# Kernel tuning notes

Hardware: AMD Instinct MI355X
Metric: run time of the kernel (lower is better)

Reference implementation:

```python
import jax, jax.numpy as jnp
import numpy as np

N_NODES = 100000
N_EDGES = 1600000
IN_CH = 256
OUT_CH = 32
HEADS = 4
NEG_SLOPE = 0.2


def setup_inputs() -> dict:
    key = jax.random.key(0)
    k1, k2, k3, k4, k5 = jax.random.split(key, 5)
    x = jax.random.normal(k1, (N_NODES, IN_CH), dtype=jnp.float32)
    edge_index = jax.random.randint(k2, (2, N_EDGES), 0, N_NODES, dtype=jnp.int64)
    hc = HEADS * OUT_CH
    # glorot init like the torch module
    std_w = np.sqrt(6.0 / (hc + IN_CH))
    W = jax.random.uniform(k3, (hc, IN_CH), dtype=jnp.float32, minval=-std_w, maxval=std_w)
    b = jnp.zeros((hc,), dtype=jnp.float32)
    std_a = np.sqrt(6.0 / (hc + 2))
    att = jax.random.uniform(k4, (hc, 2), dtype=jnp.float32, minval=-std_a, maxval=std_a)
    return {"x": x, "edge_index": edge_index, "W": W, "b": b, "att": att}


def reference(x, edge_index, W, b, att):
    # flow = 'target_to_source': tid=0, sid=1
    tar = edge_index[0]
    src = edge_index[1]
    feat = x @ W.T + b                      # [N, H*C]
    e_pre = feat @ att                      # [N, 2]
    e_src = e_pre[:, 0:1]                   # [N, 1]
    e_tar = e_pre[:, 1:2]                   # [N, 1]
    # edge scores
    e = jnp.exp(jax.nn.leaky_relu(e_src[src] + e_tar[tar], negative_slope=NEG_SLOPE))   # [E, 1]
    e_self = jnp.exp(jax.nn.leaky_relu(e_src + e_tar, negative_slope=NEG_SLOPE))        # [N, 1]
    # softmax denominator over incoming edges + self loop
    e_sum = jax.ops.segment_sum(e, tar, num_segments=N_NODES) + e_self                  # [N, 1]
    alpha_self = e_self / e_sum             # [N, 1]
    alpha = e / e_sum[tar]                  # [E, 1]
    # weighted aggregation (dropout=0 / eval -> identity)
    out = jax.ops.segment_sum(feat[src] * alpha, tar, num_segments=N_NODES)
    out = out + feat * alpha_self           # [N, H*C], concat=True
    return out
```

## Files before the change

kernel.cpp:

```cpp
#include <hip/hip_runtime.h>
#include <hip/hip_bf16.h>
#include <math.h>

#define N_NODES 100000
#define N_EDGES 1600000
#define IN_CH 256
#define HC 128
#define NEG_SLOPE 0.2f

#define NB_C 196
#define CCAP 8704
#define CHUNK 3200

typedef __attribute__((ext_vector_type(8))) short short8;
typedef __attribute__((ext_vector_type(4))) float floatx4;

__device__ inline ushort f2b(float f) {
    __hip_bfloat16 h = __float2bfloat16(f);
    return *(ushort*)&h;
}

#define GBM 128

__global__ __launch_bounds__(256, 2)
void gemm_mfma(const float* __restrict__ x, const float* __restrict__ W,
               const float* __restrict__ b, const float* __restrict__ att,
               __hip_bfloat16* __restrict__ featb,
               float* __restrict__ e_src, float* __restrict__ e_tar,
               float* __restrict__ e_self) {
    __shared__ ushort xs[128][72];
    __shared__ ushort wsh[128][72];

    const int tid  = threadIdx.x;
    const int wave = tid >> 6;
    const int lane = tid & 63;
    const int l16  = lane >> 4;
    const int lc   = lane & 15;
    const int row0 = blockIdx.x * GBM;

    floatx4 acc[2][8];
    #pragma unroll
    for (int mt = 0; mt < 2; ++mt)
        #pragma unroll
        for (int nt = 0; nt < 8; ++nt)
            acc[mt][nt] = (floatx4){0.f, 0.f, 0.f, 0.f};

    for (int kb = 0; kb < 4; ++kb) {
        const int r  = tid >> 4;
        const int kq = tid & 15;
        #pragma unroll
        for (int i = 0; i < 8; ++i) {
            int rr = r + i * 16;
            int gr = row0 + rr;
            float4 v = make_float4(0.f, 0.f, 0.f, 0.f);
            if (gr < N_NODES)
                v = *(const float4*)&x[(size_t)gr * IN_CH + kb * 64 + kq * 4];
            ushort4 u;
            u.x = f2b(v.x); u.y = f2b(v.y); u.z = f2b(v.z); u.w = f2b(v.w);
            *(ushort4*)&xs[rr][kq * 4] = u;
        }
        #pragma unroll
        for (int i = 0; i < 8; ++i) {
            int rr = r + i * 16;
            float4 v = *(const float4*)&W[(size_t)rr * IN_CH + kb * 64 + kq * 4];
            ushort4 u;
            u.x = f2b(v.x); u.y = f2b(v.y); u.z = f2b(v.z); u.w = f2b(v.w);
            *(ushort4*)&wsh[rr][kq * 4] = u;
        }
        __syncthreads();
        #pragma unroll
        for (int ks = 0; ks < 2; ++ks) {
            short8 a0 = *(short8*)&xs[wave * 32 + lc][ks * 32 + l16 * 8];
            short8 a1 = *(short8*)&xs[wave * 32 + 16 + lc][ks * 32 + l16 * 8];
            short8 bf[8];
            #pragma unroll
            for (int nt = 0; nt < 8; ++nt)
                bf[nt] = *(short8*)&wsh[nt * 16 + lc][ks * 32 + l16 * 8];
            #pragma unroll
            for (int nt = 0; nt < 8; ++nt) {
                acc[0][nt] = __builtin_amdgcn_mfma_f32_16x16x32_bf16(a0, bf[nt], acc[0][nt], 0, 0, 0);
                acc[1][nt] = __builtin_amdgcn_mfma_f32_16x16x32_bf16(a1, bf[nt], acc[1][nt], 0, 0, 0);
            }
        }
        __syncthreads();
    }

    float av0[8], av1[8], bc[8];
    #pragma unroll
    for (int nt = 0; nt < 8; ++nt) {
        float2 av = *(const float2*)&att[(nt * 16 + lc) * 2];
        av0[nt] = av.x; av1[nt] = av.y;
        bc[nt] = b[nt * 16 + lc];
    }

    #pragma unroll
    for (int mt = 0; mt < 2; ++mt) {
        #pragma unroll
        for (int rg = 0; rg < 4; ++rg) {
            int row = row0 + wave * 32 + mt * 16 + l16 * 4 + rg;
            float s = 0.f, t = 0.f;
            float vals[8];
            #pragma unroll
            for (int nt = 0; nt < 8; ++nt) {
                float v = acc[mt][nt][rg] + bc[nt];
                vals[nt] = v;
                s += v * av0[nt];
                t += v * av1[nt];
            }
            #pragma unroll
            for (int off = 8; off; off >>= 1) {
                s += __shfl_xor(s, off);
                t += __shfl_xor(t, off);
            }
            if (row < N_NODES) {
                if (lc == 0) {
                    e_src[row] = s;
                    e_tar[row] = t;
                    float z = s + t;
                    float lr = z > 0.f ? z : NEG_SLOPE * z;
                    e_self[row] = __expf(lr);
                }
                #pragma unroll
                for (int nt = 0; nt < 8; ++nt)
                    featb[(size_t)row * HC + nt * 16 + lc] = __float2bfloat16(vals[nt]);
            }
        }
    }
}

__global__ __launch_bounds__(256)
void bin2_k(const int* __restrict__ ei, int* __restrict__ gcur,
            int* __restrict__ ebuf) {
    __shared__ int lcnt[NB_C];
    __shared__ int lcur[NB_C];
    const int base = blockIdx.x * CHUNK;

    for (int i = threadIdx.x; i < NB_C; i += 256) lcnt[i] = 0;
    __syncthreads();

    for (int i = threadIdx.x; i < CHUNK; i += 256)
        atomicAdd(&lcnt[ei[base + i] >> 9], 1);
    __syncthreads();

    for (int bkt = threadIdx.x; bkt < NB_C; bkt += 256) {
        int c = lcnt[bkt];
        lcur[bkt] = c ? atomicAdd(&gcur[bkt], c) : 0;
    }
    __syncthreads();

    for (int i = threadIdx.x; i < CHUNK; i += 256) {
        int t = ei[base + i];
        int s = ei[N_EDGES + base + i];
        int bkt = t >> 9;
        int pos = atomicAdd(&lcur[bkt], 1);
        if (pos < CCAP)
            ebuf[bkt * CCAP + pos] = s | ((t & 511) << 17);
    }
}

__global__ __launch_bounds__(512)
void bucket_csr2_k(const int* __restrict__ gcur, const int* __restrict__ ebuf,
                   int* __restrict__ offsets, int* __restrict__ csr_src) {
    const int b = blockIdx.x;
    const int tid = threadIdx.x;

    __shared__ int sc[256];
    __shared__ int lcnt[512];
    __shared__ int lofs[512];
    __shared__ int lout[CCAP];

    if (tid < 256) {
        int c = 0;
        if (tid < NB_C) { c = gcur[tid]; if (c > CCAP) c = CCAP; }
        sc[tid] = c;
    }
    lcnt[tid] = 0;
    __syncthreads();
    #pragma unroll
    for (int off = 1; off < 256; off <<= 1) {
        int v = 0;
        if (tid < 256) v = sc[tid] + ((tid >= off) ? sc[tid - off] : 0);
        __syncthreads();
        if (tid < 256) sc[tid] = v;
        __syncthreads();
    }
    int count = gcur[b]; if (count > CCAP) count = CCAP;
    const int base = (b == 0) ? 0 : sc[b - 1];

    const int* st = &ebuf[b * CCAP];
    for (int i = tid; i < count; i += 512)
        atomicAdd(&lcnt[st[i] >> 17], 1);
    __syncthreads();

    lofs[tid] = lcnt[tid];
    __syncthreads();
    for (int off = 1; off < 512; off <<= 1) {
        int v = lofs[tid] + ((tid >= off) ? lofs[tid - off] : 0);
        __syncthreads();
        lofs[tid] = v;
        __syncthreads();
    }
    int excl = lofs[tid] - lcnt[tid];
    lcnt[tid] = excl;

    {
        int n0 = b * 512 + tid;
        if (n0 < N_NODES) offsets[n0] = base + excl;
    }
    if (b == NB_C - 1 && tid == 0) offsets[N_NODES] = base + count;
    __syncthreads();

    for (int i = tid; i < count; i += 512) {
        int v = st[i];
        int pos = atomicAdd(&lcnt[v >> 17], 1);
        lout[pos] = v & 0x1FFFF;
    }
    __syncthreads();

    for (int i = tid; i < count; i += 512)
        csr_src[base + i] = lout[i];
}

__device__ inline float edge_e(float z) {
    float lr = z > 0.f ? z : NEG_SLOPE * z;
    return __expf(lr);
}

__global__ __launch_bounds__(256)
void aggregate_k(const int* __restrict__ offsets, const int* __restrict__ csr_src,
                 const float* __restrict__ e_src, const float* __restrict__ e_tar,
                 const __hip_bfloat162* __restrict__ featb,
                 const float* __restrict__ e_self, float* __restrict__ out) {
    int node = blockIdx.x * 4 + (threadIdx.x >> 6);
    if (node >= N_NODES) return;
    int lane = threadIdx.x & 63;
    int beg = offsets[node];
    int end = offsets[node + 1];
    float et = e_tar[node];
    float eself = e_self[node];

    float2 fs = __bfloat1622float2(featb[(size_t)node * 64 + lane]);
    float esum = eself;
    float accx = eself * fs.x, accy = eself * fs.y;

    int j = beg;
    int npeel = (4 - (j & 3)) & 3;
    if (npeel > end - j) npeel = end - j;
    for (int p = 0; p < npeel; ++p, ++j) {
        int s0 = csr_src[j];
        float e0 = edge_e(e_src[s0] + et);
        float2 f0 = __bfloat1622float2(featb[(size_t)s0 * 64 + lane]);
        esum += e0; accx += e0 * f0.x; accy += e0 * f0.y;
    }

    for (; j + 7 < end; j += 8) {
        int4 a = *(const int4*)&csr_src[j];
        int4 c = *(const int4*)&csr_src[j + 4];
        float p0 = e_src[a.x], p1 = e_src[a.y], p2 = e_src[a.z], p3 = e_src[a.w];
        float p4 = e_src[c.x], p5 = e_src[c.y], p6 = e_src[c.z], p7 = e_src[c.w];
        float2 f0 = __bfloat1622float2(featb[(size_t)a.x * 64 + lane]);
        float2 f1 = __bfloat1622float2(featb[(size_t)a.y * 64 + lane]);
        float2 f2 = __bfloat1622float2(featb[(size_t)a.z * 64 + lane]);
        float2 f3 = __bfloat1622float2(featb[(size_t)a.w * 64 + lane]);
        float2 f4 = __bfloat1622float2(featb[(size_t)c.x * 64 + lane]);
        float2 f5 = __bfloat1622float2(featb[(size_t)c.y * 64 + lane]);
        float2 f6 = __bfloat1622float2(featb[(size_t)c.z * 64 + lane]);
        float2 f7 = __bfloat1622float2(featb[(size_t)c.w * 64 + lane]);
        float e0 = edge_e(p0 + et), e1 = edge_e(p1 + et);
        float e2 = edge_e(p2 + et), e3 = edge_e(p3 + et);
        float e4 = edge_e(p4 + et), e5 = edge_e(p5 + et);
        float e6 = edge_e(p6 + et), e7 = edge_e(p7 + et);
        esum += ((e0 + e1) + (e2 + e3)) + ((e4 + e5) + (e6 + e7));
        accx += e0 * f0.x + e1 * f1.x + e2 * f2.x + e3 * f3.x;
        accx += e4 * f4.x + e5 * f5.x + e6 * f6.x + e7 * f7.x;
        accy += e0 * f0.y + e1 * f1.y + e2 * f2.y + e3 * f3.y;
        accy += e4 * f4.y + e5 * f5.y + e6 * f6.y + e7 * f7.y;
    }
    for (; j + 3 < end; j += 4) {
        int4 a = *(const int4*)&csr_src[j];
        float p0 = e_src[a.x], p1 = e_src[a.y], p2 = e_src[a.z], p3 = e_src[a.w];
        float2 f0 = __bfloat1622float2(featb[(size_t)a.x * 64 + lane]);
        float2 f1 = __bfloat1622float2(featb[(size_t)a.y * 64 + lane]);
        float2 f2 = __bfloat1622float2(featb[(size_t)a.z * 64 + lane]);
        float2 f3 = __bfloat1622float2(featb[(size_t)a.w * 64 + lane]);
        float e0 = edge_e(p0 + et), e1 = edge_e(p1 + et);
        float e2 = edge_e(p2 + et), e3 = edge_e(p3 + et);
        esum += (e0 + e1) + (e2 + e3);
        accx += e0 * f0.x + e1 * f1.x + e2 * f2.x + e3 * f3.x;
        accy += e0 * f0.y + e1 * f1.y + e2 * f2.y + e3 * f3.y;
    }
    for (; j < end; ++j) {
        int s0 = csr_src[j];
        float e0 = edge_e(e_src[s0] + et);
        float2 f0 = __bfloat1622float2(featb[(size_t)s0 * 64 + lane]);
        esum += e0;
        accx += e0 * f0.x;
        accy += e0 * f0.y;
    }
    float inv = 1.f / esum;
    *(float2*)&out[(size_t)node * HC + lane * 2] = make_float2(accx * inv, accy * inv);
}

extern "C" void kernel_launch(void* const* d_in, const int* in_sizes, int n_in,
                              void* d_out, int out_size, void* d_ws, size_t ws_size,
                              hipStream_t stream) {
    const float* x   = (const float*)d_in[0];
    const int*   ei  = (const int*)d_in[1];
    const float* W   = (const float*)d_in[2];
    const float* b   = (const float*)d_in[3];
    const float* att = (const float*)d_in[4];
    float* out = (float*)d_out;

    unsigned char* p = (unsigned char*)d_ws;
    auto take = [&](size_t bytes) {
        unsigned char* r = p;
        p += (bytes + 255) & ~(size_t)255;
        return (void*)r;
    };
    __hip_bfloat16* featb = (__hip_bfloat16*)take((size_t)N_NODES * HC * sizeof(__hip_bfloat16));
    float* e_src   = (float*)take((size_t)N_NODES * sizeof(float));
    float* e_tar   = (float*)take((size_t)N_NODES * sizeof(float));
    float* e_self  = (float*)take((size_t)N_NODES * sizeof(float));
    int*   offsets = (int*)take((size_t)(N_NODES + 1) * sizeof(int));
    int*   gcur    = (int*)take((size_t)NB_C * sizeof(int));
    int*   csr_src = (int*)take((size_t)N_EDGES * sizeof(int));
    int*   ebuf    = (int*)take((size_t)NB_C * CCAP * sizeof(int));

    (void)hipMemsetAsync(gcur, 0, NB_C * sizeof(int), stream);

    bin2_k<<<N_EDGES / CHUNK, 256, 0, stream>>>(ei, gcur, ebuf);
    bucket_csr2_k<<<NB_C, 512, 0, stream>>>(gcur, ebuf, offsets, csr_src);

    gemm_mfma<<<(N_NODES + GBM - 1) / GBM, 256, 0, stream>>>(x, W, b, att, featb,
                                                             e_src, e_tar, e_self);

    aggregate_k<<<(N_NODES + 3) / 4, 256, 0, stream>>>(offsets, csr_src, e_src, e_tar,
                                                       (const __hip_bfloat162*)featb,
                                                       e_self, out);
}
```

Before: 303.5 us.

## Precompute per-edge attention weights in CSR build kernel

Moves the GEMM ahead of the edge binning so the CSR bucket kernel can compute each edge's exp(leaky_relu(e_src+e_tar)) and store it in a new per-edge weight array alongside csr_src. The aggregation kernel then reads the weights contiguously as float4 instead of gathering e_src per edge and recomputing exp. The aim is to cut the random gathers and the transcendental work in the hot aggregation loop. In exchange it adds a 6.4 MB write plus read of the weight array, and the bucket kernel now does its own e_src gathers.

```diff
diff --git a/kernel.cpp b/kernel.cpp
--- a/kernel.cpp
+++ b/kernel.cpp
@@ -18,6 +18,11 @@
 __device__ inline ushort f2b(float f) {
     __hip_bfloat16 h = __float2bfloat16(f);
     return *(ushort*)&h;
+}
+
+__device__ inline float edge_e(float z) {
+    float lr = z > 0.f ? z : NEG_SLOPE * z;
+    return __expf(lr);
 }
 
 #define GBM 128
@@ -160,7 +165,9 @@
 
 __global__ __launch_bounds__(512)
 void bucket_csr2_k(const int* __restrict__ gcur, const int* __restrict__ ebuf,
-                   int* __restrict__ offsets, int* __restrict__ csr_src) {
+                   const float* __restrict__ e_src, const float* __restrict__ e_tar,
+                   int* __restrict__ offsets, int* __restrict__ csr_src,
+                   float* __restrict__ ewb) {
     const int b = blockIdx.x;
     const int tid = threadIdx.x;
 
@@ -168,6 +175,12 @@
     __shared__ int lcnt[512];
     __shared__ int lofs[512];
     __shared__ int lout[CCAP];
+    __shared__ float ltar[512];
+
+    {
+        int n = b * 512 + tid;
+        ltar[tid] = (n < N_NODES) ? e_tar[n] : 0.f;
+    }
 
     if (tid < 256) {
         int c = 0;
@@ -213,22 +226,21 @@
     for (int i = tid; i < count; i += 512) {
         int v = st[i];
         int pos = atomicAdd(&lcnt[v >> 17], 1);
-        lout[pos] = v & 0x1FFFF;
-    }
-    __syncthreads();
-
-    for (int i = tid; i < count; i += 512)
-        csr_src[base + i] = lout[i];
-}
-
-__device__ inline float edge_e(float z) {
-    float lr = z > 0.f ? z : NEG_SLOPE * z;
-    return __expf(lr);
+        lout[pos] = v;
+    }
+    __syncthreads();
+
+    for (int i = tid; i < count; i += 512) {
+        int v = lout[i];
+        int src = v & 0x1FFFF;
+        csr_src[base + i] = src;
+        ewb[base + i] = edge_e(e_src[src] + ltar[v >> 17]);
+    }
 }
 
 __global__ __launch_bounds__(256)
 void aggregate_k(const int* __restrict__ offsets, const int* __restrict__ csr_src,
-                 const float* __restrict__ e_src, const float* __restrict__ e_tar,
+                 const float* __restrict__ ewb,
                  const __hip_bfloat162* __restrict__ featb,
                  const float* __restrict__ e_self, float* __restrict__ out) {
     int node = blockIdx.x * 4 + (threadIdx.x >> 6);
@@ -236,7 +248,6 @@
     int lane = threadIdx.x & 63;
     int beg = offsets[node];
     int end = offsets[node + 1];
-    float et = e_tar[node];
     float eself = e_self[node];
 
     float2 fs = __bfloat1622float2(featb[(size_t)node * 64 + lane]);
@@ -248,7 +259,7 @@
     if (npeel > end - j) npeel = end - j;
     for (int p = 0; p < npeel; ++p, ++j) {
         int s0 = csr_src[j];
-        float e0 = edge_e(e_src[s0] + et);
+        float e0 = ewb[j];
         float2 f0 = __bfloat1622float2(featb[(size_t)s0 * 64 + lane]);
         esum += e0; accx += e0 * f0.x; accy += e0 * f0.y;
     }
@@ -256,8 +267,8 @@
     for (; j + 7 < end; j += 8) {
         int4 a = *(const int4*)&csr_src[j];
         int4 c = *(const int4*)&csr_src[j + 4];
-        float p0 = e_src[a.x], p1 = e_src[a.y], p2 = e_src[a.z], p3 = e_src[a.w];
-        float p4 = e_src[c.x], p5 = e_src[c.y], p6 = e_src[c.z], p7 = e_src[c.w];
+        float4 eA = *(const float4*)&ewb[j];
+        float4 eB = *(const float4*)&ewb[j + 4];
         float2 f0 = __bfloat1622float2(featb[(size_t)a.x * 64 + lane]);
         float2 f1 = __bfloat1622float2(featb[(size_t)a.y * 64 + lane]);
         float2 f2 = __bfloat1622float2(featb[(size_t)a.z * 64 + lane]);
@@ -266,32 +277,26 @@
         float2 f5 = __bfloat1622float2(featb[(size_t)c.y * 64 + lane]);
         float2 f6 = __bfloat1622float2(featb[(size_t)c.z * 64 + lane]);
         float2 f7 = __bfloat1622float2(featb[(size_t)c.w * 64 + lane]);
-        float e0 = edge_e(p0 + et), e1 = edge_e(p1 + et);
-        float e2 = edge_e(p2 + et), e3 = edge_e(p3 + et);
-        float e4 = edge_e(p4 + et), e5 = edge_e(p5 + et);
-        float e6 = edge_e(p6 + et), e7 = edge_e(p7 + et);
-        esum += ((e0 + e1) + (e2 + e3)) + ((e4 + e5) + (e6 + e7));
-        accx += e0 * f0.x + e1 * f1.x + e2 * f2.x + e3 * f3.x;
-        accx += e4 * f4.x + e5 * f5.x + e6 * f6.x + e7 * f7.x;
-        accy += e0 * f0.y + e1 * f1.y + e2 * f2.y + e3 * f3.y;
-        accy += e4 * f4.y + e5 * f5.y + e6 * f6.y + e7 * f7.y;
+        esum += ((eA.x + eA.y) + (eA.z + eA.w)) + ((eB.x + eB.y) + (eB.z + eB.w));
+        accx += eA.x * f0.x + eA.y * f1.x + eA.z * f2.x + eA.w * f3.x;
+        accx += eB.x * f4.x + eB.y * f5.x + eB.z * f6.x + eB.w * f7.x;
+        accy += eA.x * f0.y + eA.y * f1.y + eA.z * f2.y + eA.w * f3.y;
+        accy += eB.x * f4.y + eB.y * f5.y + eB.z * f6.y + eB.w * f7.y;
     }
     for (; j + 3 < end; j += 4) {
         int4 a = *(const int4*)&csr_src[j];
-        float p0 = e_src[a.x], p1 = e_src[a.y], p2 = e_src[a.z], p3 = e_src[a.w];
+        float4 eA = *(const float4*)&ewb[j];
         float2 f0 = __bfloat1622float2(featb[(size_t)a.x * 64 + lane]);
         float2 f1 = __bfloat1622float2(featb[(size_t)a.y * 64 + lane]);
         float2 f2 = __bfloat1622float2(featb[(size_t)a.z * 64 + lane]);
         float2 f3 = __bfloat1622float2(featb[(size_t)a.w * 64 + lane]);
-        float e0 = edge_e(p0 + et), e1 = edge_e(p1 + et);
-        float e2 = edge_e(p2 + et), e3 = edge_e(p3 + et);
-        esum += (e0 + e1) + (e2 + e3);
-        accx += e0 * f0.x + e1 * f1.x + e2 * f2.x + e3 * f3.x;
-        accy += e0 * f0.y + e1 * f1.y + e2 * f2.y + e3 * f3.y;
+        esum += (eA.x + eA.y) + (eA.z + eA.w);
+        accx += eA.x * f0.x + eA.y * f1.x + eA.z * f2.x + eA.w * f3.x;
+        accy += eA.x * f0.y + eA.y * f1.y + eA.z * f2.y + eA.w * f3.y;
     }
     for (; j < end; ++j) {
         int s0 = csr_src[j];
-        float e0 = edge_e(e_src[s0] + et);
+        float e0 = ewb[j];
         float2 f0 = __bfloat1622float2(featb[(size_t)s0 * 64 + lane]);
         esum += e0;
         accx += e0 * f0.x;
@@ -324,17 +329,19 @@
     int*   offsets = (int*)take((size_t)(N_NODES + 1) * sizeof(int));
     int*   gcur    = (int*)take((size_t)NB_C * sizeof(int));
     int*   csr_src = (int*)take((size_t)N_EDGES * sizeof(int));
+    float* ewb     = (float*)take((size_t)N_EDGES * sizeof(float));
     int*   ebuf    = (int*)take((size_t)NB_C * CCAP * sizeof(int));
 
     (void)hipMemsetAsync(gcur, 0, NB_C * sizeof(int), stream);
-
-    bin2_k<<<N_EDGES / CHUNK, 256, 0, stream>>>(ei, gcur, ebuf);
-    bucket_csr2_k<<<NB_C, 512, 0, stream>>>(gcur, ebuf, offsets, csr_src);
 
     gemm_mfma<<<(N_NODES + GBM - 1) / GBM, 256, 0, stream>>>(x, W, b, att, featb,
                                                              e_src, e_tar, e_self);
 
-    aggregate_k<<<(N_NODES + 3) / 4, 256, 0, stream>>>(offsets, csr_src, e_src, e_tar,
+    bin2_k<<<N_EDGES / CHUNK, 256, 0, stream>>>(ei, gcur, ebuf);
+    bucket_csr2_k<<<NB_C, 512, 0, stream>>>(gcur, ebuf, e_src, e_tar,
+                                            offsets, csr_src, ewb);
+
+    aggregate_k<<<(N_NODES + 3) / 4, 256, 0, stream>>>(offsets, csr_src, ewb,
                                                        (const __hip_bfloat162*)featb,
                                                        e_self, out);
 }
```

Measured after the change: 306.0 us. About the same (+0.8%).
